# Optimization experiments

Hardware: AMD Instinct MI355X
Metric: run time of the kernel (lower is better)

The kernel has to match this reference:

```python
import jax
import jax.numpy as jnp
import numpy as np

# ---- static config (mirrors ReduceMask.__init__ / get_block_params) ----
N, H, W = 32, 1024, 1024
BH, BW = 16, 16            # block_size (pool window)
KH, KW = 3, 3              # kernel_size
SH, SW = 1, 1              # stride
PH, PW = KH // 2, KW // 2  # symmetric padding = 1,1
BSH, BSW = BH - KH + SH, BW - KW + SW   # block_stride = 14,14
BCH = (H + 2 * PH - BH) // BSH + 1      # block_cnt h = 73
BCW = (W + 2 * PW - BW) // BSW + 1      # block_cnt w = 73
THRESHOLD = 0.9
TOTAL = N * BCH * BCW      # fixed upper bound on number of active blocks


def setup_inputs() -> dict:
    key = jax.random.key(0)
    mask = jax.random.uniform(key, (N, 1, H, W), dtype=jnp.float32)
    return {"mask": mask}


def reference(mask):
    # pad H,W by kernel_size//2 (constant zeros), as in F.pad(mask, padding)
    x = jnp.pad(mask, ((0, 0), (0, 0), (PH, PH), (PW, PW)))
    # max_pool2d with window=block_size, stride=block_stride, padding=0
    pooled = jax.lax.reduce_window(
        x, -jnp.inf, jax.lax.max,
        window_dimensions=(1, 1, BH, BW),
        window_strides=(1, 1, BSH, BSW),
        padding='VALID',
    )[:, 0]  # squeeze channel -> [N, BCH, BCW]
    active = pooled > THRESHOLD
    # torch.nonzero -> row-major (n, bh, bw) indices; fixed-size padded with -1 for jit
    nz = jnp.nonzero(active, size=TOTAL, fill_value=-1)
    return jnp.stack(nz, axis=1).astype(jnp.int32)  # [TOTAL, 3]
```

## Files before the change

kernel.cpp:

```cpp
#include <hip/hip_runtime.h>

#define NI    32
#define HH    1024
#define WW    1024
#define BHW   16
#define BS    14
#define NBH   73
#define NBW   73
#define NCHUNK (NI * NBH)
#define TOTAL  (NI * NBH * NBW)

struct umask2 { unsigned long long x, y; };

__device__ __forceinline__ float4 max4(float4 a, float4 b) {
    return make_float4(fmaxf(a.x, b.x), fmaxf(a.y, b.y),
                       fmaxf(a.z, b.z), fmaxf(a.w, b.w));
}

__global__ __launch_bounds__(256, 4) void pool_kernel(const float* __restrict__ mask,
                                                      umask2* __restrict__ masks,
                                                      int* __restrict__ counts) {
    const int chunk = blockIdx.x;
    const int n  = chunk / NBH;
    const int by = chunk % NBH;
    const int tid = threadIdx.x;

    __shared__ float colmax[WW];
    __shared__ unsigned long long sm0, sm1;

    const int r0 = by * BS - 1;
    const int rs = max(r0, 0);
    const float* p = mask + (size_t)n * HH * WW + (size_t)rs * WW + tid * 4;

    float4 m = *(const float4*)p;
    #pragma unroll
    for (int dr = 1; dr < 15; ++dr)
        m = max4(m, *(const float4*)(p + (size_t)dr * WW));
    if (by > 0)
        m = max4(m, *(const float4*)(p + (size_t)15 * WW));

    const int c = tid * 4;
    colmax[c + 0] = m.x;
    colmax[c + 1] = m.y;
    colmax[c + 2] = m.z;
    colmax[c + 3] = m.w;
    __syncthreads();

    int f = 0;
    if (tid < NBW) {
        const int c0 = tid * BS - 1;
        float mx = colmax[max(c0, 0)];
        #pragma unroll
        for (int dc = 1; dc < BHW; ++dc) mx = fmaxf(mx, colmax[c0 + dc]);
        f = (mx > 0.9f) ? 1 : 0;
    }
    const unsigned long long b = __ballot(f);
    const int wave = tid >> 6;
    const int lane = tid & 63;
    if (wave == 0 && lane == 0) sm0 = b;
    if (wave == 1 && lane == 0) sm1 = b;
    __syncthreads();
    if (tid == 0) {
        umask2 mm; mm.x = sm0; mm.y = sm1;
        masks[chunk] = mm;
        counts[chunk] = __popcll(sm0) + __popcll(sm1);
    }
}

__global__ __launch_bounds__(128) void scatter_kernel(const umask2* __restrict__ masks,
                                                      const int* __restrict__ counts,
                                                      int* __restrict__ out) {
    const int chunk = blockIdx.x;
    const int n  = chunk / NBH;
    const int by = chunk % NBH;
    const int tid  = threadIdx.x;
    const int lane = tid & 63;
    const int wave = tid >> 6;

    __shared__ int wsum[2];

    int partial = 0;
    for (int i = tid; i < chunk; i += 128) partial += counts[i];
    #pragma unroll
    for (int off = 32; off > 0; off >>= 1) partial += __shfl_down(partial, off, 64);
    if (lane == 0) wsum[wave] = partial;

    const umask2 m = masks[chunk];
    __syncthreads();
    const int e = wsum[0] + wsum[1];
    const int c = __popcll(m.x) + __popcll(m.y);

    if (tid < NBW) {
        int f, prefix;
        if (wave == 0) {
            f = (int)((m.x >> tid) & 1ull);
            prefix = __popcll(m.x & ((1ull << tid) - 1ull));
        } else {
            const int t = tid - 64;
            f = (int)((m.y >> t) & 1ull);
            prefix = __popcll(m.x) + __popcll(m.y & ((1ull << t) - 1ull));
        }
        if (f) {
            const int pos = e + prefix;
            out[3 * pos + 0] = n;
            out[3 * pos + 1] = by;
            out[3 * pos + 2] = tid;
        }
    }

    const int slack = NBW - c;
    if (slack > 0) {
        const int s_incl = (chunk + 1) * NBW - (e + c);
        const int base3 = 3 * (TOTAL - s_incl);
        const int n3 = 3 * slack;
        for (int i = tid; i < n3; i += 128) out[base3 + i] = -1;
    }
}

extern "C" void kernel_launch(void* const* d_in, const int* in_sizes, int n_in,
                              void* d_out, int out_size, void* d_ws, size_t ws_size,
                              hipStream_t stream) {
    const float* mask = (const float*)d_in[0];
    int* out = (int*)d_out;

    umask2* masks = (umask2*)d_ws;
    int* counts = (int*)(masks + NCHUNK);

    pool_kernel<<<NCHUNK, 256, 0, stream>>>(mask, masks, counts);
    scatter_kernel<<<NCHUNK, 128, 0, stream>>>(masks, counts, out);
}
```

Baseline: 190.8 us.

## Early-exit row reduction once all pooled blocks exceed threshold

Reads the pool window rows two at a time. After each pair, a block-wide ballot checks whether every output block in the chunk already has an inside-window float4 whose value exceeds the threshold. If so, it writes an all-ones mask and skips the remaining row loads. This is meant to cut global memory traffic when activations are dense. In exchange it adds per-iteration barriers, and the loads become serialised.

```diff
diff --git a/kernel.cpp b/kernel.cpp
--- a/kernel.cpp
+++ b/kernel.cpp
@@ -23,21 +23,60 @@
     const int chunk = blockIdx.x;
     const int n  = chunk / NBH;
     const int by = chunk % NBH;
-    const int tid = threadIdx.x;
+    const int tid  = threadIdx.x;
+    const int lane = tid & 63;
+    const int wave = tid >> 6;
 
     __shared__ float colmax[WW];
+    __shared__ unsigned long long wb[4];
+    __shared__ int sdone[4];
     __shared__ unsigned long long sm0, sm1;
 
     const int r0 = by * BS - 1;
     const int rs = max(r0, 0);
+    const int nr = (by > 0) ? 16 : 15;
     const float* p = mask + (size_t)n * HH * WW + (size_t)rs * WW + tid * 4;
 
-    float4 m = *(const float4*)p;
-    #pragma unroll
-    for (int dr = 1; dr < 15; ++dr)
-        m = max4(m, *(const float4*)(p + (size_t)dr * WW));
-    if (by > 0)
-        m = max4(m, *(const float4*)(p + (size_t)15 * WW));
+    float4 m = make_float4(-1e30f, -1e30f, -1e30f, -1e30f);
+    bool done = false;
+
+    for (int k = 0; k < 8 && !done; ++k) {
+        const int r1 = 2 * k, r2 = 2 * k + 1;
+        m = max4(m, *(const float4*)(p + (size_t)r1 * WW));
+        if (r2 < nr)
+            m = max4(m, *(const float4*)(p + (size_t)r2 * WW));
+
+        const float mm = fmaxf(fmaxf(m.x, m.y), fmaxf(m.z, m.w));
+        const unsigned long long bal = __ballot(mm > 0.9f);
+        if (lane == 0) wb[wave] = bal;
+        __syncthreads();
+
+        bool whit = true;
+        if (tid < NBW) {
+            const int c0 = tid * BS;
+            const int lo = (c0 + 2) >> 2;
+            const int hi = (c0 + 11) >> 2;
+            const int w0 = lo >> 6, sh = lo & 63;
+            unsigned long long bits = wb[w0] >> sh;
+            if (w0 < 3 && sh) bits |= wb[w0 + 1] << (64 - sh);
+            const int nb = hi - lo + 1;
+            whit = (bits & ((1ull << nb) - 1ull)) != 0ull;
+        }
+        const unsigned long long miss = __ballot(!whit);
+        if (lane == 0) sdone[wave] = (miss == 0ull);
+        __syncthreads();
+        done = (sdone[0] & sdone[1] & sdone[2] & sdone[3]) != 0;
+        __syncthreads();
+    }
+
+    if (done) {
+        if (tid == 0) {
+            umask2 mmk; mmk.x = ~0ull; mmk.y = (1ull << (NBW - 64)) - 1ull;
+            masks[chunk] = mmk;
+            counts[chunk] = NBW;
+        }
+        return;
+    }
 
     const int c = tid * 4;
     colmax[c + 0] = m.x;
@@ -55,14 +94,12 @@
         f = (mx > 0.9f) ? 1 : 0;
     }
     const unsigned long long b = __ballot(f);
-    const int wave = tid >> 6;
-    const int lane = tid & 63;
     if (wave == 0 && lane == 0) sm0 = b;
     if (wave == 1 && lane == 0) sm1 = b;
     __syncthreads();
     if (tid == 0) {
-        umask2 mm; mm.x = sm0; mm.y = sm1;
-        masks[chunk] = mm;
+        umask2 mm2; mm2.x = sm0; mm2.y = sm1;
+        masks[chunk] = mm2;
         counts[chunk] = __popcll(sm0) + __popcll(sm1);
     }
 }
```

New measurement: 177.9 us. 6.8% less time.
